# Optimization experiments

Measured on AMD Instinct MI355X. Metric: run time of the kernel, lower is better.

## Reference

```python
import jax, jax.numpy as jnp
import numpy as np
import math

D_K = 64
EPS = 1e-6  # module fills masked scores with eps, not -inf


def setup_inputs() -> dict:
    key = jax.random.key(0)
    k1, k2, k3, k4 = jax.random.split(key, 4)
    BH, S, D = 64, 1024, D_K
    q_matrix = jax.random.normal(k1, (BH, S, D), dtype=jnp.float32)
    k_matrix = jax.random.normal(k2, (BH, S, D), dtype=jnp.float32)
    v_matrix = jax.random.normal(k3, (BH, S, D), dtype=jnp.float32)
    mask = jax.random.randint(k4, (S, S), 0, 2, dtype=jnp.int32)
    return {"q_matrix": q_matrix, "k_matrix": k_matrix, "v_matrix": v_matrix, "mask": mask}


def reference(q_matrix, k_matrix, v_matrix, mask):
    scale = math.sqrt(D_K)
    # scores: [BH, S, S]
    scores = jnp.einsum('bqd,bkd->bqk', q_matrix, k_matrix) / scale
    # masked_fill(mask == 0, eps) -- mask broadcasts over batch dim
    scores = jnp.where(mask == 0, jnp.float32(EPS), scores)
    attention = jax.nn.softmax(scores, axis=-1)
    result = jnp.einsum('bqk,bkd->bqd', attention, v_matrix)
    return result
```

## Files before the change

kernel.cpp:

```cpp
#include <hip/hip_runtime.h>

#define BH 64
#define SEQ 1024
#define DH 64
#define EPSV 1e-6f
#define MFIX 8.3f
#define EPSC (EPSV - MFIX)

typedef short short8 __attribute__((ext_vector_type(8)));
typedef float f32x4 __attribute__((ext_vector_type(4)));
typedef float f32x16 __attribute__((ext_vector_type(16)));
typedef unsigned u32x4 __attribute__((ext_vector_type(4)));
typedef unsigned short u16;
typedef unsigned short u16x4 __attribute__((ext_vector_type(4)));

__device__ __forceinline__ u16 f2bf(float x) {
    unsigned u = __builtin_bit_cast(unsigned, x);
    u += 0x7fffu + ((u >> 16) & 1u);
    return (u16)(u >> 16);
}
__device__ __forceinline__ void gload16(const void* g, void* l) {
    __builtin_amdgcn_global_load_lds(
        (const __attribute__((address_space(1))) void*)g,
        (__attribute__((address_space(3))) void*)l, 16, 0, 0);
}

__global__ __launch_bounds__(256) void prep_all(
        const float* __restrict__ kf, const float* __restrict__ vf,
        const int* __restrict__ mask,
        u16* __restrict__ kb16, u16* __restrict__ vt, unsigned* __restrict__ bits) {
    __shared__ u16 tile[64][65];
    const int b = blockIdx.x;
    const int t = threadIdx.x;
    if (b < 1024) {
        const int bh = b >> 4;
        const int st = b & 15;
        const int sl = t >> 2, c = t & 3;
        const float* src = vf + ((size_t)bh * SEQ + st * 64 + sl) * DH + c * 16;
#pragma unroll
        for (int q = 0; q < 4; ++q) {
            f32x4 x = *(const f32x4*)(src + q * 4);
#pragma unroll
            for (int j = 0; j < 4; ++j) tile[sl][c * 16 + q * 4 + j] = f2bf(x[j]);
        }
        __syncthreads();
        const int d = t >> 2, scn = t & 3;
        u16* dst = vt + ((size_t)bh * DH + d) * SEQ + st * 64 + scn * 16;
        short8 o0, o1;
#pragma unroll
        for (int j = 0; j < 8; ++j) o0[j] = (short)tile[scn * 16 + j][d];
#pragma unroll
        for (int j = 0; j < 8; ++j) o1[j] = (short)tile[scn * 16 + 8 + j][d];
        *(short8*)dst = o0;
        *(short8*)(dst + 8) = o1;
    } else if (b < 2048) {
        const size_t base = ((size_t)(b - 1024) * 256 + t) * 16;
#pragma unroll
        for (int j = 0; j < 4; ++j) {
            f32x4 x = *(const f32x4*)(kf + base + j * 4);
            u16x4 o;
#pragma unroll
            for (int i = 0; i < 4; ++i) o[i] = f2bf(x[i]);
            *(u16x4*)(kb16 + base + j * 4) = o;
        }
    } else {
        const int tt = (b - 2048) * 256 + t;
        const int qr = tt >> 5, w = tt & 31;
        const int* src = mask + (size_t)qr * SEQ + w * 32;
        unsigned bb = 0;
#pragma unroll
        for (int j = 0; j < 32; ++j) bb |= (src[j] != 0 ? 1u : 0u) << j;
        bits[tt] = bb;
    }
}


#define STAGE(T, BUF) do { \
    const size_t bo_ = (size_t)(BUF) * 16384; \
    const size_t tk_ = (size_t)(T) << 12; \
    const size_t tv_ = (size_t)(T) << 6; \
    gload16(ks0 + tk_, sd0 + bo_); \
    gload16(vs0 + tv_, sd1 + bo_); \
    gload16(ks1 + tk_, sd2 + bo_); \
    gload16(vs1 + tv_, sd3 + bo_); \
} while (0)

#define ITER(T, MWC, MWN) do { \
    asm volatile("s_waitcnt vmcnt(0)" ::: "memory"); \
    __builtin_amdgcn_sched_barrier(0); \
    __builtin_amdgcn_s_barrier(); \
    __builtin_amdgcn_sched_barrier(0); \
    MWN = mp[mbase + (((T) + 1 < 16) ? (T) + 1 : 15)]; \
    if ((T) < 15) STAGE((T) + 1, ((T) + 1) & 1); \
    const char* bb_ = (const char*)smem + (size_t)((T) & 1) * 16384; \
    short8 kc0_ = *(const short8*)(bb_ + koff[0]); \
    short8 kc1_ = *(const short8*)(bb_ + koff[1]); \
    short8 kc2_ = *(const short8*)(bb_ + koff[2]); \
    short8 kc3_ = *(const short8*)(bb_ + koff[3]); \
    f32x16 sn_; \
    _Pragma("unroll") \
    for (int z_ = 0; z_ < 16; ++z_) sn_[z_] = 0.f; \
    __builtin_amdgcn_s_setprio(1); \
    sn_ = __builtin_amdgcn_mfma_f32_32x32x16_bf16(kc0_, bqh0, sn_, 0, 0, 0); \
    sn_ = __builtin_amdgcn_mfma_f32_32x32x16_bf16(kc1_, bqh1, sn_, 0, 0, 0); \
    sn_ = __builtin_amdgcn_mfma_f32_32x32x16_bf16(kc2_, bqh2, sn_, 0, 0, 0); \
    sn_ = __builtin_amdgcn_mfma_f32_32x32x16_bf16(kc3_, bqh3, sn_, 0, 0, 0); \
    __builtin_amdgcn_s_setprio(0); \
    const unsigned wm_ = (MWC) >> (hi << 2); \
    float p_[16]; \
    _Pragma("unroll") \
    for (int r_ = 0; r_ < 16; ++r_) { \
        float arg_ = fmaf(sn_[r_], 0.125f, -MFIX); \
        arg_ = ((wm_ >> ((r_ & 3) + ((r_ >> 2) << 3))) & 1u) ? arg_ : EPSC; \
        p_[r_] = __expf(arg_); \
    } \
    ls += (((p_[0] + p_[1]) + (p_[2] + p_[3])) + ((p_[4] + p_[5]) + (p_[6] + p_[7]))) \
        + (((p_[8] + p_[9]) + (p_[10] + p_[11])) + ((p_[12] + p_[13]) + (p_[14] + p_[15]))); \
    unsigned x0_, x1_, y0_, y1_, x2_, x3_, y2_, y3_; \
    asm("v_cvt_pk_bf16_f32 %0, %1, %2" : "=v"(x0_) : "v"(p_[0]),  "v"(p_[1])); \
    asm("v_cvt_pk_bf16_f32 %0, %1, %2" : "=v"(x1_) : "v"(p_[2]),  "v"(p_[3])); \
    asm("v_cvt_pk_bf16_f32 %0, %1, %2" : "=v"(y0_) : "v"(p_[4]),  "v"(p_[5])); \
    asm("v_cvt_pk_bf16_f32 %0, %1, %2" : "=v"(y1_) : "v"(p_[6]),  "v"(p_[7])); \
    asm volatile("v_permlane32_swap_b32 %0, %1" : "+v"(x0_), "+v"(y0_)); \
    asm volatile("v_permlane32_swap_b32 %0, %1" : "+v"(x1_), "+v"(y1_)); \
    u32x4 pw0_; pw0_[0] = x0_; pw0_[1] = x1_; pw0_[2] = y0_; pw0_[3] = y1_; \
    short8 pa0_ = __builtin_bit_cast(short8, pw0_); \
    asm("v_cvt_pk_bf16_f32 %0, %1, %2" : "=v"(x2_) : "v"(p_[8]),  "v"(p_[9])); \
    asm("v_cvt_pk_bf16_f32 %0, %1, %2" : "=v"(x3_) : "v"(p_[10]), "v"(p_[11])); \
    asm("v_cvt_pk_bf16_f32 %0, %1, %2" : "=v"(y2_) : "v"(p_[12]), "v"(p_[13])); \
    asm("v_cvt_pk_bf16_f32 %0, %1, %2" : "=v"(y3_) : "v"(p_[14]), "v"(p_[15])); \
    asm volatile("v_permlane32_swap_b32 %0, %1" : "+v"(x2_), "+v"(y2_)); \
    asm volatile("v_permlane32_swap_b32 %0, %1" : "+v"(x3_), "+v"(y3_)); \
    u32x4 pw1_; pw1_[0] = x2_; pw1_[1] = x3_; pw1_[2] = y2_; pw1_[3] = y3_; \
    short8 pa1_ = __builtin_bit_cast(short8, pw1_); \
    short8 v00_ = *(const short8*)(bb_ + voff0[0]); \
    short8 v01_ = *(const short8*)(bb_ + voff0[1]); \
    short8 v10_ = *(const short8*)(bb_ + voff1[0]); \
    short8 v11_ = *(const short8*)(bb_ + voff1[1]); \
    __builtin_amdgcn_s_setprio(1); \
    O0 = __builtin_amdgcn_mfma_f32_32x32x16_bf16(pa0_, v00_, O0, 0, 0, 0); \
    O0 = __builtin_amdgcn_mfma_f32_32x32x16_bf16(pa1_, v01_, O0, 0, 0, 0); \
    O1 = __builtin_amdgcn_mfma_f32_32x32x16_bf16(pa0_, v10_, O1, 0, 0, 0); \
    O1 = __builtin_amdgcn_mfma_f32_32x32x16_bf16(pa1_, v11_, O1, 0, 0, 0); \
    __builtin_amdgcn_s_setprio(0); \
} while (0)

__global__ __launch_bounds__(256, 4) void attn_main(
        const float* __restrict__ q, const u16* __restrict__ kb16,
        const u16* __restrict__ vt, const unsigned* __restrict__ mbits,
        float* __restrict__ out) {
    __shared__ __align__(16) unsigned char smem[2 * 16384];

    const int t = threadIdx.x;
    const int lane = t & 63;
    const int wave = t >> 6;
    const int l5 = lane & 31;
    const int hi = lane >> 5;
    const int wq = wave & 1;
    const int half = wave >> 1;

    const int bid = blockIdx.x;
    const int bh = ((bid & 7) << 3) | ((bid >> 3) & 7);
    const int qb = bid >> 6;
    const int qrow0 = qb * 64 + wq * 32;

    const float* qp = q + ((size_t)bh * SEQ + qrow0 + l5) * DH + hi * 8;
    short8 bqh0, bqh1, bqh2, bqh3;
    {
        short8 hh[4];
#pragma unroll
        for (int c = 0; c < 4; ++c) {
            f32x4 x0 = *(const f32x4*)(qp + c * 16);
            f32x4 x1 = *(const f32x4*)(qp + c * 16 + 4);
#pragma unroll
            for (int j = 0; j < 4; ++j) {
                hh[c][j] = (short)f2bf(x0[j]);
                hh[c][4 + j] = (short)f2bf(x1[j]);
            }
        }
        bqh0 = hh[0]; bqh1 = hh[1]; bqh2 = hh[2]; bqh3 = hh[3];
    }

    const char* kg = (const char*)(kb16 + (size_t)bh * SEQ * DH);
    const char* vg = (const char*)(vt + (size_t)bh * DH * SEQ);
    const char* ks0 = kg + (size_t)(t >> 3) * 128 + (size_t)(((t & 7) ^ ((t >> 3) & 7)) << 4);
    const char* ks1 = ks0 + 512 * 128;
    const char* vs0 = vg + (size_t)(t >> 2) * (SEQ * 2) + (size_t)(((t & 3) ^ ((t >> 3) & 3)) << 4);
    const char* vs1 = vs0 + 512 * 2;
    char* sd0 = (char*)smem + wave * 1024;
    char* sd1 = sd0 + 4096;
    char* sd2 = sd0 + 8192;
    char* sd3 = sd0 + 12288;

    const int hb = half * 8192;
    int koff[4], voff0[2], voff1[2];
#pragma unroll
    for (int c = 0; c < 4; ++c)
        koff[c] = hb + l5 * 128 + ((((c << 1) | hi) ^ (l5 & 7)) << 4);
#pragma unroll
    for (int c = 0; c < 2; ++c) {
        const int s = (((c << 1) | hi) ^ ((l5 >> 1) & 3)) << 4;
        voff0[c] = hb + 4096 + l5 * 64 + s;
        voff1[c] = hb + 4096 + (32 + l5) * 64 + s;
    }

    const unsigned* mp = mbits + (size_t)(qrow0 + l5) * 32;
    const int mbase = half * 16;

    f32x16 O0, O1;
#pragma unroll
    for (int r = 0; r < 16; ++r) { O0[r] = 0.f; O1[r] = 0.f; }
    float ls = 0.f;

    unsigned mwA = mp[mbase], mwB;
    STAGE(0, 0);

#pragma unroll 1
    for (int tt = 0; tt < 14; tt += 2) {
        ITER(tt,     mwA, mwB);
        ITER(tt + 1, mwB, mwA);
    }
    ITER(14, mwA, mwB);
    ITER(15, mwB, mwA);

    const float lsh = ls + __shfl_xor(ls, 32);
    __syncthreads();
    float* lsums = (float*)smem;
    float* osc   = (float*)((char*)smem + 512);
    if (hi == 0) lsums[(wq * 2 + half) * 32 + l5] = lsh;
    if (wave >= 2) {
        float* dst = osc + ((size_t)(wq * 64) + lane) * 33;
#pragma unroll
        for (int r = 0; r < 16; ++r) { dst[r] = O0[r]; dst[16 + r] = O1[r]; }
    }
    __syncthreads();
    if (wave < 2) {
        const float* src = osc + ((size_t)(wq * 64) + lane) * 33;
        const float* lrow = lsums + wq * 64;
        float* op = out + ((size_t)bh * SEQ + qrow0) * DH;
#pragma unroll
        for (int r = 0; r < 16; ++r) {
            const int qr = (r & 3) + ((r >> 2) << 3) + (hi << 2);
            const float iv = 1.f / (lrow[qr] + lrow[32 + qr]);
            op[(size_t)qr * DH + l5]      = (O0[r] + src[r]) * iv;
            op[(size_t)qr * DH + 32 + l5] = (O1[r] + src[16 + r]) * iv;
        }
    }
}

extern "C" void kernel_launch(void* const* d_in, const int* in_sizes, int n_in,
                              void* d_out, int out_size, void* d_ws, size_t ws_size,
                              hipStream_t stream) {
    const float* q = (const float*)d_in[0];
    const float* k = (const float*)d_in[1];
    const float* v = (const float*)d_in[2];
    const int* mask = (const int*)d_in[3];
    float* out = (float*)d_out;

    char* w = (char*)d_ws;
    const size_t NQ = (size_t)BH * SEQ * DH;
    u16* kb16 = (u16*)(w);
    u16* vt = (u16*)(w + 2 * NQ);
    unsigned* mbits = (unsigned*)(w + 4 * NQ);

    prep_all<<<dim3(2176), dim3(256), 0, stream>>>(k, v, mask, kb16, vt, mbits);
    attn_main<<<dim3(1024), dim3(256), 0, stream>>>(q, kb16, vt, mbits, out);
}
```

Baseline: 50.88 us.

## Compute softmax row sums via MFMA, use exp2, preload mask words, fully unroll

```diff
diff --git a/kernel.cpp b/kernel.cpp
--- a/kernel.cpp
+++ b/kernel.cpp
@@ -5,7 +5,10 @@
 #define DH 64
 #define EPSV 1e-6f
 #define MFIX 8.3f
-#define EPSC (EPSV - MFIX)
+#define LOG2E 1.44269504088896f
+#define SCALE2 (0.125f * LOG2E)
+#define MFIX2 (MFIX * LOG2E)
+#define EPSC2 ((EPSV - MFIX) * LOG2E)
 
 typedef short short8 __attribute__((ext_vector_type(8)));
 typedef float f32x4 __attribute__((ext_vector_type(4)));
@@ -85,12 +88,11 @@
     gload16(vs1 + tv_, sd3 + bo_); \
 } while (0)
 
-#define ITER(T, MWC, MWN) do { \
+#define ITER(T) do { \
     asm volatile("s_waitcnt vmcnt(0)" ::: "memory"); \
     __builtin_amdgcn_sched_barrier(0); \
     __builtin_amdgcn_s_barrier(); \
     __builtin_amdgcn_sched_barrier(0); \
-    MWN = mp[mbase + (((T) + 1 < 16) ? (T) + 1 : 15)]; \
     if ((T) < 15) STAGE((T) + 1, ((T) + 1) & 1); \
     const char* bb_ = (const char*)smem + (size_t)((T) & 1) * 16384; \
     short8 kc0_ = *(const short8*)(bb_ + koff[0]); \
@@ -106,16 +108,14 @@
     sn_ = __builtin_amdgcn_mfma_f32_32x32x16_bf16(kc2_, bqh2, sn_, 0, 0, 0); \
     sn_ = __builtin_amdgcn_mfma_f32_32x32x16_bf16(kc3_, bqh3, sn_, 0, 0, 0); \
     __builtin_amdgcn_s_setprio(0); \
-    const unsigned wm_ = (MWC) >> (hi << 2); \
+    const unsigned wm_ = mwAll[(T)] >> (hi << 2); \
     float p_[16]; \
     _Pragma("unroll") \
     for (int r_ = 0; r_ < 16; ++r_) { \
-        float arg_ = fmaf(sn_[r_], 0.125f, -MFIX); \
-        arg_ = ((wm_ >> ((r_ & 3) + ((r_ >> 2) << 3))) & 1u) ? arg_ : EPSC; \
-        p_[r_] = __expf(arg_); \
+        float arg_ = fmaf(sn_[r_], SCALE2, -MFIX2); \
+        arg_ = ((wm_ >> ((r_ & 3) + ((r_ >> 2) << 3))) & 1u) ? arg_ : EPSC2; \
+        p_[r_] = __builtin_exp2f(arg_); \
     } \
-    ls += (((p_[0] + p_[1]) + (p_[2] + p_[3])) + ((p_[4] + p_[5]) + (p_[6] + p_[7]))) \
-        + (((p_[8] + p_[9]) + (p_[10] + p_[11])) + ((p_[12] + p_[13]) + (p_[14] + p_[15]))); \
     unsigned x0_, x1_, y0_, y1_, x2_, x3_, y2_, y3_; \
     asm("v_cvt_pk_bf16_f32 %0, %1, %2" : "=v"(x0_) : "v"(p_[0]),  "v"(p_[1])); \
     asm("v_cvt_pk_bf16_f32 %0, %1, %2" : "=v"(x1_) : "v"(p_[2]),  "v"(p_[3])); \
@@ -142,6 +142,8 @@
     O0 = __builtin_amdgcn_mfma_f32_32x32x16_bf16(pa1_, v01_, O0, 0, 0, 0); \
     O1 = __builtin_amdgcn_mfma_f32_32x32x16_bf16(pa0_, v10_, O1, 0, 0, 0); \
     O1 = __builtin_amdgcn_mfma_f32_32x32x16_bf16(pa1_, v11_, O1, 0, 0, 0); \
+    LS = __builtin_amdgcn_mfma_f32_32x32x16_bf16(pa0_, bones, LS, 0, 0, 0); \
+    LS = __builtin_amdgcn_mfma_f32_32x32x16_bf16(pa1_, bones, LS, 0, 0, 0); \
     __builtin_amdgcn_s_setprio(0); \
 } while (0)
 
@@ -204,44 +206,40 @@
         voff1[c] = hb + 4096 + (32 + l5) * 64 + s;
     }
 
-    const unsigned* mp = mbits + (size_t)(qrow0 + l5) * 32;
-    const int mbase = half * 16;
-
-    f32x16 O0, O1;
-#pragma unroll
-    for (int r = 0; r < 16; ++r) { O0[r] = 0.f; O1[r] = 0.f; }
-    float ls = 0.f;
-
-    unsigned mwA = mp[mbase], mwB;
+    const unsigned* mp = mbits + (size_t)(qrow0 + l5) * 32 + half * 16;
+    unsigned mwAll[16];
+#pragma unroll
+    for (int tt = 0; tt < 16; ++tt) mwAll[tt] = mp[tt];
+
+    f32x16 O0, O1, LS;
+#pragma unroll
+    for (int r = 0; r < 16; ++r) { O0[r] = 0.f; O1[r] = 0.f; LS[r] = 0.f; }
+    short8 bones;
+#pragma unroll
+    for (int j = 0; j < 8; ++j) bones[j] = (short)0x3F80;
+
     STAGE(0, 0);
 
-#pragma unroll 1
-    for (int tt = 0; tt < 14; tt += 2) {
-        ITER(tt,     mwA, mwB);
-        ITER(tt + 1, mwB, mwA);
-    }
-    ITER(14, mwA, mwB);
-    ITER(15, mwB, mwA);
-
-    const float lsh = ls + __shfl_xor(ls, 32);
+    ITER(0);  ITER(1);  ITER(2);  ITER(3);
+    ITER(4);  ITER(5);  ITER(6);  ITER(7);
+    ITER(8);  ITER(9);  ITER(10); ITER(11);
+    ITER(12); ITER(13); ITER(14); ITER(15);
+
     __syncthreads();
-    float* lsums = (float*)smem;
-    float* osc   = (float*)((char*)smem + 512);
-    if (hi == 0) lsums[(wq * 2 + half) * 32 + l5] = lsh;
+    float* osc = (float*)smem;
     if (wave >= 2) {
-        float* dst = osc + ((size_t)(wq * 64) + lane) * 33;
-#pragma unroll
-        for (int r = 0; r < 16; ++r) { dst[r] = O0[r]; dst[16 + r] = O1[r]; }
+        float* dst = osc + ((size_t)(wq * 64) + lane) * 49;
+#pragma unroll
+        for (int r = 0; r < 16; ++r) { dst[r] = O0[r]; dst[16 + r] = O1[r]; dst[32 + r] = LS[r]; }
     }
     __syncthreads();
     if (wave < 2) {
-        const float* src = osc + ((size_t)(wq * 64) + lane) * 33;
-        const float* lrow = lsums + wq * 64;
+        const float* src = osc + ((size_t)(wq * 64) + lane) * 49;
         float* op = out + ((size_t)bh * SEQ + qrow0) * DH;
 #pragma unroll
         for (int r = 0; r < 16; ++r) {
             const int qr = (r & 3) + ((r >> 2) << 3) + (hi << 2);
-            const float iv = 1.f / (lrow[qr] + lrow[32 + qr]);
+            const float iv = 1.f / (LS[r] + src[32 + r]);
             op[(size_t)qr * DH + l5]      = (O0[r] + src[r]) * iv;
             op[(size_t)qr * DH + 32 + l5] = (O1[r] + src[16 + r]) * iv;
         }
```

Result: slower. 59.28 us (+16.5%).
